# Performance work log

Measured on AMD Instinct MI355X. Metric: run time of the kernel, lower is better.

The kernel has to match this reference:

```python
import jax, jax.numpy as jnp
import numpy as np

D, H, HD, F, A, P, NB, MD = 1024, 16, 64, 2816, 64, 30, 32, 128
B, L = 4, 1024


def _rel_bucket(rel, num_buckets=NB, max_distance=MD):
    # T5 relative position bucket, bidirectional=False (decoder self-attn)
    rel = -jnp.minimum(rel, 0)
    max_exact = num_buckets // 2
    is_small = rel < max_exact
    large = max_exact + (
        jnp.log(jnp.maximum(rel, 1).astype(jnp.float32) / max_exact)
        / np.log(max_distance / max_exact)
        * (num_buckets - max_exact)
    ).astype(jnp.int32)
    large = jnp.minimum(large, num_buckets - 1)
    return jnp.where(is_small, rel, large)


def _rmsnorm(x, scale, eps=1e-6):
    var = jnp.mean(jnp.square(x), axis=-1, keepdims=True)
    return x * jax.lax.rsqrt(var + eps) * scale


def _attn(x, kv, wq, wk, wv, wo, mask, bias, pk, pv):
    # x: [B,Lq,D], kv: [B,Lk,D], prefix pk/pv: [B,P,H,HD]
    hd = wq.shape[-1]
    q = jnp.einsum('bqd,dhe->bqhe', x, wq) * (hd ** -0.5)
    k = jnp.einsum('bkd,dhe->bkhe', kv, wk)
    v = jnp.einsum('bkd,dhe->bkhe', kv, wv)
    k = jnp.concatenate([pk, k], axis=1)  # prefix KV prepended
    v = jnp.concatenate([pv, v], axis=1)
    logits = jnp.einsum('bqhe,bkhe->bhqk', q, k).astype(jnp.float32)
    p = pk.shape[1]
    if bias is not None:
        logits = logits + jnp.pad(bias, ((0, 0), (0, 0), (0, 0), (p, 0)))
    mask = jnp.pad(mask, ((0, 0), (0, 0), (0, 0), (p, 0)), constant_values=True)
    logits = jnp.where(mask, logits, jnp.float32(-1e10))
    w = jax.nn.softmax(logits, axis=-1).astype(x.dtype)
    o = jnp.einsum('bhqk,bkhe->bqhe', w, v)
    return jnp.einsum('bqhe,hed->bqd', o, wo)


def setup_inputs() -> dict:
    key = jax.random.key(0)
    ks = jax.random.split(key, 24)
    s = D ** -0.5
    inp = {
        'inputs': jax.random.normal(ks[0], (B, L, D), jnp.float32),
        'encoded': jax.random.normal(ks[1], (B, L, D), jnp.float32),
        'adapter_wd': jax.random.normal(ks[2], (B, D, A), jnp.float32) * s,
        'adapter_wu': jax.random.normal(ks[3], (B, A, D), jnp.float32) * (A ** -0.5),
        'adapter_bd': jax.random.normal(ks[4], (B, A), jnp.float32) * 0.02,
        'adapter_bu': jax.random.normal(ks[5], (B, D), jnp.float32) * 0.02,
        'prefix_key': jax.random.normal(ks[6], (B, 2, P, H, HD), jnp.float32),
        'prefix_value': jax.random.normal(ks[7], (B, 2, P, H, HD), jnp.float32),
        'ln1': jnp.ones((D,), jnp.float32),
        'ln2': jnp.ones((D,), jnp.float32),
        'ln3': jnp.ones((D,), jnp.float32),
        'sa_wq': jax.random.normal(ks[8], (D, H, HD), jnp.float32) * s,
        'sa_wk': jax.random.normal(ks[9], (D, H, HD), jnp.float32) * s,
        'sa_wv': jax.random.normal(ks[10], (D, H, HD), jnp.float32) * s,
        'sa_wo': jax.random.normal(ks[11], (H, HD, D), jnp.float32) * s,
        'ca_wq': jax.random.normal(ks[12], (D, H, HD), jnp.float32) * s,
        'ca_wk': jax.random.normal(ks[13], (D, H, HD), jnp.float32) * s,
        'ca_wv': jax.random.normal(ks[14], (D, H, HD), jnp.float32) * s,
        'ca_wo': jax.random.normal(ks[15], (H, HD, D), jnp.float32) * s,
        'relpos': jax.random.normal(ks[16], (H, NB), jnp.float32) * 0.1,
        'mlp_wi0': jax.random.normal(ks[17], (D, F), jnp.float32) * s,
        'mlp_wi1': jax.random.normal(ks[18], (D, F), jnp.float32) * s,
        'mlp_wo': jax.random.normal(ks[19], (F, D), jnp.float32) * (F ** -0.5),
        'decoder_mask': jnp.broadcast_to(jnp.tril(jnp.ones((L, L), bool))[None, None], (B, 1, L, L)),
        'encoder_decoder_mask': jnp.ones((B, 1, L, L), bool),
    }
    return inp


def reference(inputs, encoded, adapter_wd, adapter_wu, adapter_bd, adapter_bu,
              prefix_key, prefix_value, ln1, ln2, ln3,
              sa_wq, sa_wk, sa_wv, sa_wo, ca_wq, ca_wk, ca_wv, ca_wo,
              relpos, mlp_wi0, mlp_wi1, mlp_wo,
              decoder_mask, encoder_decoder_mask):
    l = inputs.shape[1]
    pos = jnp.arange(l)
    buckets = _rel_bucket(pos[None, :] - pos[:, None])  # [L,L]
    bias = relpos[:, buckets][None]                      # [1,H,L,L]
    # self-attention with prefix + relative bias
    x = _rmsnorm(inputs, ln1)
    x = _attn(x, x, sa_wq, sa_wk, sa_wv, sa_wo, decoder_mask, bias,
              prefix_key[:, 0], prefix_value[:, 0])
    x = x + inputs
    # cross-attention with prefix
    y = _rmsnorm(x, ln2)
    y = _attn(y, encoded, ca_wq, ca_wk, ca_wv, ca_wo, encoder_decoder_mask, None,
              prefix_key[:, 1], prefix_value[:, 1])
    y = y + x
    # gated-gelu MLP + per-example adapter
    lz = _rmsnorm(y, ln3)
    z = (jax.nn.gelu(lz @ mlp_wi0) * (lz @ mlp_wi1)) @ mlp_wo
    az = jnp.einsum('bld,bda->bla', lz, adapter_wd) + adapter_bd[:, None]
    az = jax.nn.gelu(az)
    az = jnp.einsum('bla,bad->bld', az, adapter_wu) + adapter_bu[:, None]
    z = z + az
    return z + y
```

## Files before the change

kernel.cpp:

```cpp
#include <hip/hip_runtime.h>

typedef unsigned short u16;
typedef __attribute__((ext_vector_type(8))) __bf16 bf16x8;
typedef __attribute__((ext_vector_type(4))) float f32x4;

__device__ __forceinline__ float bf2f(u16 u) {
  union { unsigned int i; float f; } v; v.i = ((unsigned int)u) << 16; return v.f;
}
__device__ __forceinline__ u16 f2bf(float f) {
  unsigned int x = __float_as_uint(f);
  unsigned int r = (x + 0x7fffu + ((x >> 16) & 1u)) >> 16;
  return (u16)r;
}
__device__ __forceinline__ u16 f2bf_fast(float f) {
  return (u16)((__float_as_uint(f) + 0x8000u) >> 16);
}
__device__ __forceinline__ float gelu_f(float x) {
  float u = 0.7978845608028654f * (x + 0.044715f * x * x * x);
  float t = 1.0f - 2.0f / (__expf(2.0f * u) + 1.0f);
  return 0.5f * x * (1.0f + t);
}
__device__ __forceinline__ void gl_lds16(const u16* g, u16* l) {
  __builtin_amdgcn_global_load_lds(
      (const __attribute__((address_space(1))) unsigned int*)g,
      (__attribute__((address_space(3))) unsigned int*)l, 16, 0, 0);
}

__global__ __launch_bounds__(256) void cast_bf16_k(const float* __restrict__ in,
                                                   u16* __restrict__ out, int n4) {
  int i = blockIdx.x * 256 + threadIdx.x;
  if (i >= n4) return;
  float4 v = ((const float4*)in)[i];
  ushort4 o;
  o.x = f2bf(v.x); o.y = f2bf(v.y); o.z = f2bf(v.z); o.w = f2bf(v.w);
  ((ushort4*)out)[i] = o;
}

__global__ __launch_bounds__(256) void transpose_k(
    const float* __restrict__ in, u16* __restrict__ out, int R, int C,
    long isb, long osb, int rs, int roff) {
  __shared__ u16 tile[32][33];
  in += (size_t)blockIdx.z * isb;
  out += (size_t)blockIdx.z * osb;
  int c0 = blockIdx.x * 32, r0 = blockIdx.y * 32;
  int tx = threadIdx.x & 31, ty = threadIdx.x >> 5;
#pragma unroll
  for (int i = 0; i < 4; ++i) {
    int rr = r0 + ty + i * 8;
    if (rr < R && c0 + tx < C) tile[ty + i * 8][tx] = f2bf(in[(size_t)rr * C + c0 + tx]);
  }
  __syncthreads();
#pragma unroll
  for (int i = 0; i < 4; ++i) {
    int cc = c0 + ty + i * 8;
    if (cc < C && r0 + tx < R)
      out[(size_t)(cc * rs + roff) * R + r0 + tx] = tile[tx][ty + i * 8];
  }
}

__global__ __launch_bounds__(256) void bias_tab_k(const float* __restrict__ relpos,
                                                  float* __restrict__ tab) {
  int idx = blockIdx.x * 256 + threadIdx.x;
  int h = idx >> 10, d = idx & 1023;
  int bucket;
  if (d < 16) bucket = d;
  else {
    int lb = 16 + (int)(logf((float)d * (1.0f / 16.0f)) * (16.0f / logf(8.0f)));
    bucket = lb < 31 ? lb : 31;
  }
  tab[idx] = relpos[h * 32 + bucket];
}

__global__ __launch_bounds__(256) void prefix_fill_k(
    const float* __restrict__ pK, const float* __restrict__ pV,
    u16* __restrict__ Kd, u16* __restrict__ Vtd, int sSel) {
  int idx = blockIdx.x * 256 + threadIdx.x;
  int e = idx & 63, p = (idx >> 6) & 31, h = (idx >> 11) & 15, b = idx >> 15;
  int key = (p < 30) ? p : (1024 + p);
  float kv = 0.f, vv = 0.f;
  if (p < 30) {
    size_t src = ((((size_t)(b * 2 + sSel)) * 30 + p) * 16 + h) * 64 + e;
    kv = pK[src]; vv = pV[src];
  }
  Kd[(((size_t)(b * 16 + h)) * 1056 + key) * 64 + e] = f2bf(kv);
  Vtd[(((size_t)(b * 16 + h)) * 64 + e) * 1056 + key] = f2bf(vv);
}

__global__ __launch_bounds__(256) void rmsnorm_k(const float* __restrict__ in,
                                                 const float* __restrict__ scale,
                                                 u16* __restrict__ out) {
  const int D = 1024;
  size_t base = (size_t)blockIdx.x * D;
  int t = threadIdx.x;
  float x[4];
#pragma unroll
  for (int i = 0; i < 4; ++i) x[i] = in[base + t + i * 256];
  float s = x[0] * x[0] + x[1] * x[1] + x[2] * x[2] + x[3] * x[3];
#pragma unroll
  for (int off = 1; off < 64; off <<= 1) s += __shfl_xor(s, off, 64);
  __shared__ float ws4[4];
  if ((t & 63) == 0) ws4[t >> 6] = s;
  __syncthreads();
  float tot = ws4[0] + ws4[1] + ws4[2] + ws4[3];
  float r = rsqrtf(tot * (1.0f / D) + 1e-6f);
#pragma unroll
  for (int i = 0; i < 4; ++i) {
    int c = t + i * 256;
    out[base + c] = f2bf(x[i] * r * scale[c]);
  }
}

__global__ __launch_bounds__(256) void rmsnorm_sum_k(
    const float* __restrict__ in0, const float* __restrict__ in1,
    const float* __restrict__ res, const float* __restrict__ scale,
    u16* __restrict__ outn, float* __restrict__ outs) {
  const int D = 1024;
  size_t base = (size_t)blockIdx.x * D;
  int t = threadIdx.x;
  float x[4];
#pragma unroll
  for (int i = 0; i < 4; ++i) {
    int c = t + i * 256;
    x[i] = in0[base + c] + in1[base + c] + res[base + c];
    outs[base + c] = x[i];
  }
  float s = x[0] * x[0] + x[1] * x[1] + x[2] * x[2] + x[3] * x[3];
#pragma unroll
  for (int off = 1; off < 64; off <<= 1) s += __shfl_xor(s, off, 64);
  __shared__ float ws4[4];
  if ((t & 63) == 0) ws4[t >> 6] = s;
  __syncthreads();
  float tot = ws4[0] + ws4[1] + ws4[2] + ws4[3];
  float r = rsqrtf(tot * (1.0f / D) + 1e-6f);
#pragma unroll
  for (int i = 0; i < 4; ++i) {
    int c = t + i * 256;
    outn[base + c] = f2bf(x[i] * r * scale[c]);
  }
}

template <int MODE>
__global__ __launch_bounds__(256) void gemm97(
    const u16* __restrict__ A, const u16* __restrict__ Bt, void* __restrict__ out,
    void* __restrict__ out2, void* __restrict__ out3,
    const float* __restrict__ res1, int M, int N, int K, int Ks, float alpha) {
  const int BK = 32;
  __shared__ __align__(16) u16 As[128 * 32];
  __shared__ __align__(16) u16 Bs[128 * 32];

  const int t = threadIdx.x;
  const int wave = t >> 6, lane = t & 63;
  int m0, n0;
  if (MODE != 13) {
    int wgid = blockIdx.y * gridDim.x + blockIdx.x;
    const int cpx = (gridDim.x * gridDim.y) >> 3;
    wgid = (wgid & 7) * cpx + (wgid >> 3);
    m0 = (wgid / gridDim.x) * 128;
    n0 = (wgid % gridDim.x) * 128;
  } else {
    m0 = blockIdx.y * 128;
    n0 = blockIdx.x * 128;
  }
  const int kbase = blockIdx.z * Ks;
  const int fr = lane & 15, fq = lane >> 4;
  const int wm = (wave >> 1) * 64, wn = (wave & 1) * 64;

  const int srow = wave * 32 + (lane >> 2);
  const int scol = (lane & 3) * 8;
  const u16* ag0 = A + (size_t)(m0 + srow) * K + kbase + scol;
  const u16* ag1 = ag0 + (size_t)16 * K;
  const u16* bg0 = Bt + (size_t)(n0 + srow) * K + kbase + scol;
  const u16* bg1 = bg0 + (size_t)16 * K;
  u16* al0 = &As[(wave * 32) * 32];
  u16* al1 = &As[(wave * 32 + 16) * 32];
  u16* bl0 = &Bs[(wave * 32) * 32];
  u16* bl1 = &Bs[(wave * 32 + 16) * 32];

  f32x4 acc[16];
#pragma unroll
  for (int i = 0; i < 16; ++i) acc[i] = (f32x4){0.f, 0.f, 0.f, 0.f};

  for (int k0 = 0; k0 < Ks; k0 += BK) {
    gl_lds16(ag0 + k0, al0);
    gl_lds16(ag1 + k0, al1);
    gl_lds16(bg0 + k0, bl0);
    gl_lds16(bg1 + k0, bl1);
    __syncthreads();
    bf16x8 af[4], bf[4];
#pragma unroll
    for (int i = 0; i < 4; ++i)
      af[i] = *(const bf16x8*)&As[(wm + i * 16 + fr) * 32 + fq * 8];
#pragma unroll
    for (int j = 0; j < 4; ++j)
      bf[j] = *(const bf16x8*)&Bs[(wn + j * 16 + fr) * 32 + fq * 8];
#pragma unroll
    for (int i = 0; i < 4; ++i)
#pragma unroll
      for (int j = 0; j < 4; ++j)
        acc[i * 4 + j] = __builtin_amdgcn_mfma_f32_16x16x32_bf16(
            af[i], bf[j], acc[i * 4 + j], 0, 0, 0);
    __syncthreads();
  }

#pragma unroll
  for (int i = 0; i < 4; ++i) {
#pragma unroll
    for (int rr = 0; rr < 4; ++rr) {
      long gm = (long)m0 + wm + i * 16 + fq * 4 + rr;
#pragma unroll
      for (int j = 0; j < 4; ++j) {
        int gn = n0 + wn + j * 16 + fr;
        float v = acc[i * 4 + j][rr];
        size_t oi = (size_t)gm * N + gn;
        if (MODE == 1) {
          float* po = blockIdx.z ? (float*)out2 : (float*)out;
          po[oi] = v;
        }
        if (MODE == 2) ((u16*)out)[oi] = f2bf(v);
        if (MODE == 8) {
          int b = (int)(gm >> 10), l = (int)(gm & 1023), h = gn >> 6, e = gn & 63;
          ((u16*)out)[(((size_t)(b * 16 + h)) * 1024 + l) * 64 + e] = f2bf(v * alpha);
        }
        if (MODE == 11) {
          int b = (int)(gm >> 10), l = (int)(gm & 1023);
          int sec = gn >> 10, nn = gn & 1023, h = nn >> 6, e = nn & 63;
          if (sec == 0)
            ((u16*)out)[(((size_t)(b * 16 + h)) * 1024 + l) * 64 + e] = f2bf(v * alpha);
          else if (sec == 1)
            ((u16*)out2)[(((size_t)(b * 16 + h)) * 1056 + 30 + l) * 64 + e] = f2bf(v);
          else
            ((u16*)out3)[(((size_t)(b * 16 + h)) * 64 + e) * 1056 + 30 + l] = f2bf(v);
        }
        if (MODE == 12) {
          int b = (int)(gm >> 10), l = (int)(gm & 1023);
          int sec = gn >> 10, nn = gn & 1023, h = nn >> 6, e = nn & 63;
          if (sec == 0)
            ((u16*)out)[(((size_t)(b * 16 + h)) * 1056 + 30 + l) * 64 + e] = f2bf(v);
          else
            ((u16*)out2)[(((size_t)(b * 16 + h)) * 64 + e) * 1056 + 30 + l] = f2bf(v);
        }
        if (MODE == 13) {
          float vo = __shfl_xor(v, 1, 64);
          if (!(fr & 1))
            ((u16*)out)[(size_t)gm * 2816 + (gn >> 1)] = f2bf(gelu_f(v) * vo);
        }
      }
    }
  }
}

template <int MODE>
__global__ __launch_bounds__(256) void gemm_bt(
    const u16* __restrict__ A, const u16* __restrict__ Bt, void* __restrict__ out,
    const float* __restrict__ res1, const float* __restrict__ res2,
    const float* __restrict__ res3, const float* __restrict__ bias,
    int M, int N, int K,
    long Asb, long Bsb, long bsb, long r1sb, long r2sb, long r3sb, long osb) {
  const int BM = 128, BK = 32, LP = 40;
  __shared__ __align__(16) u16 As[BM * LP];
  __shared__ __align__(16) u16 Bs[BM * LP];

  const int t = threadIdx.x;
  const int m0 = blockIdx.y * BM;
  const int n0 = blockIdx.x * 128;
  const int bz = blockIdx.z;
  A += (size_t)bz * Asb;
  Bt += (size_t)bz * Bsb;

  f32x4 acc[16];
#pragma unroll
  for (int i = 0; i < 16; ++i) acc[i] = (f32x4){0.f, 0.f, 0.f, 0.f};
  const int wave = t >> 6, lane = t & 63;
  const int wm = (wave >> 1) * 64, wn = (wave & 1) * 64;
  const int fr = lane & 15, fq = lane >> 4;

  for (int k0 = 0; k0 < K; k0 += BK) {
#pragma unroll
    for (int i = 0; i < 2; ++i) {
      int idx = (i * 256 + t) * 8;
      int row = idx >> 5, col = idx & 31;
      *(uint4*)&As[row * LP + col] =
          *(const uint4*)(A + (size_t)(m0 + row) * K + k0 + col);
      uint4 bv = {0u, 0u, 0u, 0u};
      if (n0 + row < N) bv = *(const uint4*)(Bt + (size_t)(n0 + row) * K + k0 + col);
      *(uint4*)&Bs[row * LP + col] = bv;
    }
    __syncthreads();
    bf16x8 af[4], bfr[4];
#pragma unroll
    for (int i = 0; i < 4; ++i)
      af[i] = *(const bf16x8*)&As[(wm + i * 16 + fr) * LP + fq * 8];
#pragma unroll
    for (int j = 0; j < 4; ++j)
      bfr[j] = *(const bf16x8*)&Bs[(wn + j * 16 + fr) * LP + fq * 8];
#pragma unroll
    for (int i = 0; i < 4; ++i)
#pragma unroll
      for (int j = 0; j < 4; ++j)
        acc[i * 4 + j] = __builtin_amdgcn_mfma_f32_16x16x32_bf16(
            af[i], bfr[j], acc[i * 4 + j], 0, 0, 0);
    __syncthreads();
  }

#pragma unroll
  for (int i = 0; i < 4; ++i) {
#pragma unroll
    for (int rr = 0; rr < 4; ++rr) {
      long gm = (long)m0 + wm + i * 16 + fq * 4 + rr;
#pragma unroll
      for (int j = 0; j < 4; ++j) {
        int gn = n0 + wn + j * 16 + fr;
        if (gn >= N) continue;
        float v = acc[i * 4 + j][rr];
        size_t oi = (size_t)bz * osb + (size_t)gm * N + gn;
        size_t ri = (size_t)gm * N + gn;
        if (MODE == 6) ((u16*)out)[oi] = f2bf(gelu_f(v + bias[(size_t)bz * bsb + gn]));
        if (MODE == 7)
          ((float*)out)[oi] = v + bias[(size_t)bz * bsb + gn] +
                              res1[(size_t)bz * r1sb + ri] +
                              res2[(size_t)bz * r2sb + ri] +
                              res3[(size_t)bz * r3sb + ri];
      }
    }
  }
}

template <bool IS_SELF>
__global__ __launch_bounds__(256) void fattn_k(
    const u16* __restrict__ Qg, const u16* __restrict__ Kg,
    const u16* __restrict__ Vtg, const float* __restrict__ bias_tab,
    u16* __restrict__ Out) {
  const int L = 1024, P = 30, KC = 1056;
  const int flat = blockIdx.x;
  const int wg = (flat & 7) * 64 + (flat >> 3);
  const int q0b = (wg & 7) * 128;
  const int h = (wg >> 3) & 15, b = wg >> 7;
  const int t = threadIdx.x, wave = t >> 6, lane = t & 63;
  const int fr = lane & 15, fq = lane >> 4;
  const int q0w = q0b + wave * 32;

  __shared__ float bTs[IS_SELF ? 1024 : 4];
  __shared__ __align__(16) u16 Ps[4][32][40];

  if (IS_SELF) {
#pragma unroll
    for (int i = 0; i < 4; ++i) bTs[t + i * 256] = bias_tab[h * 1024 + t + i * 256];
    __syncthreads();
  }

  const u16* qptr = Qg + (((size_t)(b * 16 + h)) * L + q0w + fr) * 64 + fq * 8;
  bf16x8 qa0 = *(const bf16x8*)qptr;
  bf16x8 qa1 = *(const bf16x8*)(qptr + 32);
  bf16x8 qb0 = *(const bf16x8*)(qptr + 16 * 64);
  bf16x8 qb1 = *(const bf16x8*)(qptr + 16 * 64 + 32);

  f32x4 oA[4], oB[4];
#pragma unroll
  for (int i = 0; i < 4; ++i) {
    oA[i] = (f32x4){0.f, 0.f, 0.f, 0.f};
    oB[i] = (f32x4){0.f, 0.f, 0.f, 0.f};
  }
  f32x4 olA = (f32x4){0.f, 0.f, 0.f, 0.f};
  f32x4 olB = (f32x4){0.f, 0.f, 0.f, 0.f};
  bf16x8 ones;
  {
    u16 one = 0x3F80;
#pragma unroll
    for (int i = 0; i < 8; ++i) ((u16*)&ones)[i] = one;
  }

  const int nk = IS_SELF ? (P + q0b + 128) : (P + L);
  const int nch = (nk + 31) >> 5;
  const u16* kp = Kg + ((size_t)(b * 16 + h)) * KC * 64 + (size_t)fr * 64 + fq * 8;
  const u16* vp = Vtg + ((size_t)(b * 16 + h)) * 64 * KC + (size_t)fr * KC + fq * 8;

  bf16x8 kf0 = *(const bf16x8*)(kp + 0);
  bf16x8 kf1 = *(const bf16x8*)(kp + 32);
  bf16x8 kf2 = *(const bf16x8*)(kp + 16 * 64);
  bf16x8 kf3 = *(const bf16x8*)(kp + 16 * 64 + 32);

  auto smax = [&](f32x4* s, int k0, int qoff, int rb) {
    const bool full = IS_SELF ? (k0 >= 32 && k0 + 31 - P <= qoff)
                              : (k0 + 31 < P + L);
    if (full) {
      if (IS_SELF) {
#pragma unroll
        for (int reg = 0; reg < 4; ++reg) {
          const int qq = qoff + fq * 4 + reg;
          s[0][reg] += bTs[qq - (k0 + fr - P)];
          s[1][reg] += bTs[qq - (k0 + 16 + fr - P)];
        }
      }
    } else {
#pragma unroll
      for (int reg = 0; reg < 4; ++reg) {
        const int qq = qoff + fq * 4 + reg;
#pragma unroll
        for (int t2 = 0; t2 < 2; ++t2) {
          const int kvi = k0 + t2 * 16 + fr;
          float sv = s[t2][reg];
          if (IS_SELF) {
            const int lk = kvi - P;
            if (lk >= 0) {
              if (lk <= qq) sv += bTs[qq - lk];
              else sv = -3.0e38f;
            }
          } else {
            if (kvi >= P + L) sv = -3.0e38f;
          }
          s[t2][reg] = sv;
        }
      }
    }
#pragma unroll
    for (int reg = 0; reg < 4; ++reg) {
      Ps[wave][rb + fq * 4 + reg][fr] = f2bf_fast(__expf(s[0][reg]));
      Ps[wave][rb + fq * 4 + reg][16 + fr] = f2bf_fast(__expf(s[1][reg]));
    }
  };

  for (int ch = 0; ch < nch; ++ch) {
    const int k0 = ch * 32;
    bf16x8 vf0 = *(const bf16x8*)(vp + 0 * 16 * KC + k0);
    bf16x8 vf1 = *(const bf16x8*)(vp + 1 * 16 * KC + k0);
    bf16x8 vf2 = *(const bf16x8*)(vp + 2 * 16 * KC + k0);
    bf16x8 vf3 = *(const bf16x8*)(vp + 3 * 16 * KC + k0);
    const int k0n = (ch + 1 < nch) ? (k0 + 32) : 0;
    bf16x8 kn0 = *(const bf16x8*)(kp + (size_t)k0n * 64);
    bf16x8 kn1 = *(const bf16x8*)(kp + (size_t)k0n * 64 + 32);
    bf16x8 kn2 = *(const bf16x8*)(kp + (size_t)(k0n + 16) * 64);
    bf16x8 kn3 = *(const bf16x8*)(kp + (size_t)(k0n + 16) * 64 + 32);

    f32x4 sA[2], sB[2];
    sA[0] = (f32x4){0.f, 0.f, 0.f, 0.f};
    sA[1] = (f32x4){0.f, 0.f, 0.f, 0.f};
    sB[0] = (f32x4){0.f, 0.f, 0.f, 0.f};
    sB[1] = (f32x4){0.f, 0.f, 0.f, 0.f};
    sA[0] = __builtin_amdgcn_mfma_f32_16x16x32_bf16(qa0, kf0, sA[0], 0, 0, 0);
    sA[0] = __builtin_amdgcn_mfma_f32_16x16x32_bf16(qa1, kf1, sA[0], 0, 0, 0);
    sA[1] = __builtin_amdgcn_mfma_f32_16x16x32_bf16(qa0, kf2, sA[1], 0, 0, 0);
    sA[1] = __builtin_amdgcn_mfma_f32_16x16x32_bf16(qa1, kf3, sA[1], 0, 0, 0);
    sB[0] = __builtin_amdgcn_mfma_f32_16x16x32_bf16(qb0, kf0, sB[0], 0, 0, 0);
    sB[0] = __builtin_amdgcn_mfma_f32_16x16x32_bf16(qb1, kf1, sB[0], 0, 0, 0);
    sB[1] = __builtin_amdgcn_mfma_f32_16x16x32_bf16(qb0, kf2, sB[1], 0, 0, 0);
    sB[1] = __builtin_amdgcn_mfma_f32_16x16x32_bf16(qb1, kf3, sB[1], 0, 0, 0);

    smax(sA, k0, q0w, 0);
    smax(sB, k0, q0w + 16, 16);
    __asm__ volatile("s_waitcnt lgkmcnt(0)" ::: "memory");
    bf16x8 paA = *(const bf16x8*)&Ps[wave][fr][fq * 8];
    bf16x8 paB = *(const bf16x8*)&Ps[wave][16 + fr][fq * 8];

    oA[0] = __builtin_amdgcn_mfma_f32_16x16x32_bf16(paA, vf0, oA[0], 0, 0, 0);
    oA[1] = __builtin_amdgcn_mfma_f32_16x16x32_bf16(paA, vf1, oA[1], 0, 0, 0);
    oA[2] = __builtin_amdgcn_mfma_f32_16x16x32_bf16(paA, vf2, oA[2], 0, 0, 0);
    oA[3] = __builtin_amdgcn_mfma_f32_16x16x32_bf16(paA, vf3, oA[3], 0, 0, 0);
    olA   = __builtin_amdgcn_mfma_f32_16x16x32_bf16(paA, ones, olA, 0, 0, 0);
    oB[0] = __builtin_amdgcn_mfma_f32_16x16x32_bf16(paB, vf0, oB[0], 0, 0, 0);
    oB[1] = __builtin_amdgcn_mfma_f32_16x16x32_bf16(paB, vf1, oB[1], 0, 0, 0);
    oB[2] = __builtin_amdgcn_mfma_f32_16x16x32_bf16(paB, vf2, oB[2], 0, 0, 0);
    oB[3] = __builtin_amdgcn_mfma_f32_16x16x32_bf16(paB, vf3, oB[3], 0, 0, 0);
    olB   = __builtin_amdgcn_mfma_f32_16x16x32_bf16(paB, ones, olB, 0, 0, 0);

    kf0 = kn0; kf1 = kn1; kf2 = kn2; kf3 = kn3;
  }

  float invA[4], invB[4];
#pragma unroll
  for (int reg = 0; reg < 4; ++reg) {
    invA[reg] = 1.0f / olA[reg];
    invB[reg] = 1.0f / olB[reg];
  }
#pragma unroll
  for (int dt = 0; dt < 4; ++dt) {
#pragma unroll
    for (int reg = 0; reg < 4; ++reg) {
      size_t rowA = (size_t)(b * L + q0w + fq * 4 + reg);
      Out[(rowA * 16 + h) * 64 + dt * 16 + fr] = f2bf(oA[dt][reg] * invA[reg]);
      size_t rowB = rowA + 16;
      Out[(rowB * 16 + h) * 64 + dt * 16 + fr] = f2bf(oB[dt][reg] * invB[reg]);
    }
  }
}

extern "C" void kernel_launch(void* const* d_in, const int* in_sizes, int n_in,
                              void* d_out, int out_size, void* d_ws, size_t ws_size,
                              hipStream_t stream) {
  const int B = 4, L = 1024, D = 1024, H = 16, F = 2816, AD = 64;
  const int M = B * L;
  const int KC = 1056;

  const float* inputs  = (const float*)d_in[0];
  const float* encoded = (const float*)d_in[1];
  const float* a_wd    = (const float*)d_in[2];
  const float* a_wu    = (const float*)d_in[3];
  const float* a_bd    = (const float*)d_in[4];
  const float* a_bu    = (const float*)d_in[5];
  const float* pK      = (const float*)d_in[6];
  const float* pV      = (const float*)d_in[7];
  const float* ln1     = (const float*)d_in[8];
  const float* ln2     = (const float*)d_in[9];
  const float* ln3     = (const float*)d_in[10];
  const float* sa_wq   = (const float*)d_in[11];
  const float* sa_wk   = (const float*)d_in[12];
  const float* sa_wv   = (const float*)d_in[13];
  const float* sa_wo   = (const float*)d_in[14];
  const float* ca_wq   = (const float*)d_in[15];
  const float* ca_wk   = (const float*)d_in[16];
  const float* ca_wv   = (const float*)d_in[17];
  const float* ca_wo   = (const float*)d_in[18];
  const float* relpos  = (const float*)d_in[19];
  const float* wi0     = (const float*)d_in[20];
  const float* wi1     = (const float*)d_in[21];
  const float* wom     = (const float*)d_in[22];

  char* w = (char*)d_ws;
  size_t used = 0;
  auto alloc = [&](size_t bytes) {
    char* p = w + used;
    used += (bytes + 255) & ~(size_t)255;
    return p;
  };
  u16* wqkvT  = (u16*)alloc((size_t)3072 * 1024 * 2);
  u16* woT    = (u16*)alloc((size_t)D * 1024 * 2);
  u16* cqT    = (u16*)alloc((size_t)D * 1024 * 2);
  u16* ckvT   = (u16*)alloc((size_t)2048 * 1024 * 2);
  u16* coT    = (u16*)alloc((size_t)D * 1024 * 2);
  u16* wi01T  = (u16*)alloc((size_t)5632 * 1024 * 2);
  u16* womT   = (u16*)alloc((size_t)D * F * 2);
  u16* wdT    = (u16*)alloc((size_t)B * AD * D * 2);
  u16* wuT    = (u16*)alloc((size_t)B * D * AD * 2);
  float* bT   = (float*)alloc((size_t)H * 1024 * 4);
  u16* enc16  = (u16*)alloc((size_t)M * D * 2);
  u16* xn     = (u16*)alloc((size_t)M * D * 2);
  u16* lz     = (u16*)alloc((size_t)M * D * 2);
  u16* Kc     = (u16*)alloc((size_t)B * H * KC * 64 * 2);
  u16* Vtc    = (u16*)alloc((size_t)B * H * 64 * KC * 2);
  u16* qh     = (u16*)alloc((size_t)B * H * L * 64 * 2);
  u16* ao     = (u16*)alloc((size_t)M * D * 2);
  float* xf   = (float*)alloc((size_t)M * D * 4);
  float* yf   = (float*)alloc((size_t)M * D * 4);
  u16* az1    = (u16*)alloc((size_t)B * 1024 * AD * 2);
  float* pk0  = (float*)Kc;
  u16* g      = Kc;
  float* zf0  = (float*)enc16;
  float* zf1  = (float*)ao;
  if (used > ws_size) return;

  dim3 tb(256);
  auto T = [&](const float* src, u16* dst, int R, int C, int nb, long sb,
               int rs, int roff) {
    transpose_k<<<dim3((C + 31) / 32, (R + 31) / 32, nb), tb, 0, stream>>>(
        src, dst, R, C, sb, sb, rs, roff);
  };
  T(sa_wq, wqkvT, D, 1024, 1, 0, 1, 0);
  T(sa_wk, wqkvT + (size_t)1024 * 1024, D, 1024, 1, 0, 1, 0);
  T(sa_wv, wqkvT + (size_t)2048 * 1024, D, 1024, 1, 0, 1, 0);
  T(sa_wo, woT, 1024, D, 1, 0, 1, 0);
  T(ca_wq, cqT, D, 1024, 1, 0, 1, 0);
  T(ca_wk, ckvT, D, 1024, 1, 0, 1, 0);
  T(ca_wv, ckvT + (size_t)1024 * 1024, D, 1024, 1, 0, 1, 0);
  T(ca_wo, coT, 1024, D, 1, 0, 1, 0);
  T(wi0, wi01T, D, F, 1, 0, 2, 0);
  T(wi1, wi01T, D, F, 1, 0, 2, 1);
  T(wom, womT, F, D, 1, 0, 1, 0);
  T(a_wd, wdT, D, AD, B, (long)D * AD, 1, 0);
  T(a_wu, wuT, AD, D, B, (long)AD * D, 1, 0);
  bias_tab_k<<<dim3(64), tb, 0, stream>>>(relpos, bT);
  cast_bf16_k<<<dim3(M * D / 4 / 256), tb, 0, stream>>>(encoded, enc16, M * D / 4);

#define G97(MODE, Ap, Btp, Op, O2, O3, R1, Nn, Kk, al)                         \
  gemm97<MODE><<<dim3((Nn) / 128, M / 128), tb, 0, stream>>>(                  \
      (const u16*)(Ap), (const u16*)(Btp), (void*)(Op), (void*)(O2),           \
      (void*)(O3), (const float*)(R1), M, Nn, Kk, Kk, al)

  rmsnorm_k<<<dim3(M), tb, 0, stream>>>(inputs, ln1, xn);
  G97(11, xn, wqkvT, qh, Kc, Vtc, nullptr, 3072, D, 0.125f);
  prefix_fill_k<<<dim3(512), tb, 0, stream>>>(pK, pV, Kc, Vtc, 0);
  fattn_k<true><<<dim3(512), tb, 0, stream>>>(qh, Kc, Vtc, bT, ao);
  gemm97<1><<<dim3(8, M / 128, 2), tb, 0, stream>>>(
      (const u16*)ao, (const u16*)woT, (void*)pk0, (void*)xf, nullptr,
      nullptr, M, 1024, 1024, 512, 1.f);
  rmsnorm_sum_k<<<dim3(M), tb, 0, stream>>>(pk0, xf, inputs, ln2, xn, xf);
  G97(8, xn, cqT, qh, nullptr, nullptr, nullptr, 1024, D, 0.125f);
  G97(12, enc16, ckvT, Kc, Vtc, nullptr, nullptr, 2048, D, 1.f);
  prefix_fill_k<<<dim3(512), tb, 0, stream>>>(pK, pV, Kc, Vtc, 1);
  fattn_k<false><<<dim3(512), tb, 0, stream>>>(qh, Kc, Vtc, nullptr, ao);
  gemm97<1><<<dim3(8, M / 128, 2), tb, 0, stream>>>(
      (const u16*)ao, (const u16*)coT, (void*)pk0, (void*)yf, nullptr,
      nullptr, M, 1024, 1024, 512, 1.f);
  rmsnorm_sum_k<<<dim3(M), tb, 0, stream>>>(pk0, yf, xf, ln3, lz, yf);
  gemm_bt<6><<<dim3(1, 8, B), tb, 0, stream>>>(
      lz, wdT, az1, nullptr, nullptr, nullptr, a_bd, 1024, AD, D,
      (long)1024 * D, (long)AD * D, (long)AD, 0, 0, 0, (long)1024 * AD);
  gemm97<13><<<dim3(5632 / 128, M / 128), tb, 0, stream>>>(
      (const u16*)lz, (const u16*)wi01T, (void*)g, nullptr, nullptr,
      nullptr, M, 5632, 1024, 1024, 1.f);
  gemm97<1><<<dim3(8, M / 128, 2), tb, 0, stream>>>(
      (const u16*)g, (const u16*)womT, (void*)zf0, (void*)zf1, nullptr,
      nullptr, M, 1024, 2816, 1408, 1.f);
  gemm_bt<7><<<dim3(8, 8, B), tb, 0, stream>>>(
      az1, wuT, d_out, zf0, zf1, yf, a_bu, 1024, 1024, AD,
      (long)1024 * AD, (long)D * AD, (long)1024, (long)1024 * 1024,
      (long)1024 * 1024, (long)1024 * 1024, (long)1024 * 1024);
#undef G97
  (void)in_sizes; (void)n_in; (void)out_size;
}
```

Before: 713.8 us.

## Batch weight transposes, fuse cross-attn Q/KV GEMMs, restructure gated-MLP epilogue

Replaces eight separate attention-weight transpose launches with one batched launch over a pointer table, and transposes the MLP input weights in one launch. The wi0/wi1 interleave is changed to 16-row blocks, so the gated-GELU epilogue reads gate and linear values from adjacent accumulators and no longer needs a lane shuffle. The cross-attention Q and KV projections are merged into one GEMM launch that picks its A operand per column block. Launch overhead drops, the merged GEMM fills more of the GPU, and some epilogue work goes away. The cost is that the weight layout coupling between the transpose and the MLP epilogue must stay consistent. Swizzling is now limited to MODE 1.

After: 713.8 us. Within noise of the previous version (+0.0%).

```diff
diff --git a/kernel.cpp b/kernel.cpp
--- a/kernel.cpp
+++ b/kernel.cpp
@@ -53,8 +53,36 @@
 #pragma unroll
   for (int i = 0; i < 4; ++i) {
     int cc = c0 + ty + i * 8;
-    if (cc < C && r0 + tx < R)
-      out[(size_t)(cc * rs + roff) * R + r0 + tx] = tile[tx][ty + i * 8];
+    if (cc < C && r0 + tx < R) {
+      int orow = (((cc >> 4) * rs + roff) << 4) + (cc & 15);
+      out[(size_t)orow * R + r0 + tx] = tile[tx][ty + i * 8];
+    }
+  }
+}
+
+struct TSrc8 { const float* p[8]; };
+__global__ __launch_bounds__(256) void transpose8_k(
+    TSrc8 srcs, u16* __restrict__ out, int R, int C,
+    long zstride, int rs, int roffz) {
+  __shared__ u16 tile[32][33];
+  const float* __restrict__ in = srcs.p[blockIdx.z];
+  out += (size_t)blockIdx.z * zstride;
+  const int roff = roffz ? blockIdx.z : 0;
+  int c0 = blockIdx.x * 32, r0 = blockIdx.y * 32;
+  int tx = threadIdx.x & 31, ty = threadIdx.x >> 5;
+#pragma unroll
+  for (int i = 0; i < 4; ++i) {
+    int rr = r0 + ty + i * 8;
+    if (rr < R && c0 + tx < C) tile[ty + i * 8][tx] = f2bf(in[(size_t)rr * C + c0 + tx]);
+  }
+  __syncthreads();
+#pragma unroll
+  for (int i = 0; i < 4; ++i) {
+    int cc = c0 + ty + i * 8;
+    if (cc < C && r0 + tx < R) {
+      int orow = (((cc >> 4) * rs + roff) << 4) + (cc & 15);
+      out[(size_t)orow * R + r0 + tx] = tile[tx][ty + i * 8];
+    }
   }
 }
 
@@ -141,9 +169,10 @@
 
 template <int MODE>
 __global__ __launch_bounds__(256) void gemm97(
-    const u16* __restrict__ A, const u16* __restrict__ Bt, void* __restrict__ out,
+    const u16* __restrict__ A, const u16* __restrict__ A2,
+    const u16* __restrict__ Bt, void* __restrict__ out,
     void* __restrict__ out2, void* __restrict__ out3,
-    const float* __restrict__ res1, int M, int N, int K, int Ks, float alpha) {
+    int M, int N, int K, int Ks, float alpha) {
   const int BK = 32;
   __shared__ __align__(16) u16 As[128 * 32];
   __shared__ __align__(16) u16 Bs[128 * 32];
@@ -151,7 +180,7 @@
   const int t = threadIdx.x;
   const int wave = t >> 6, lane = t & 63;
   int m0, n0;
-  if (MODE != 13) {
+  if (MODE == 1) {
     int wgid = blockIdx.y * gridDim.x + blockIdx.x;
     const int cpx = (gridDim.x * gridDim.y) >> 3;
     wgid = (wgid & 7) * cpx + (wgid >> 3);
@@ -165,9 +194,10 @@
   const int fr = lane & 15, fq = lane >> 4;
   const int wm = (wave >> 1) * 64, wn = (wave & 1) * 64;
 
+  const u16* Ause = (MODE == 14 && n0 >= 1024) ? A2 : A;
   const int srow = wave * 32 + (lane >> 2);
   const int scol = (lane & 3) * 8;
-  const u16* ag0 = A + (size_t)(m0 + srow) * K + kbase + scol;
+  const u16* ag0 = Ause + (size_t)(m0 + srow) * K + kbase + scol;
   const u16* ag1 = ag0 + (size_t)16 * K;
   const u16* bg0 = Bt + (size_t)(n0 + srow) * K + kbase + scol;
   const u16* bg1 = bg0 + (size_t)16 * K;
@@ -207,6 +237,16 @@
 #pragma unroll
     for (int rr = 0; rr < 4; ++rr) {
       long gm = (long)m0 + wm + i * 16 + fq * 4 + rr;
+      if (MODE == 13) {
+#pragma unroll
+        for (int p = 0; p < 2; ++p) {
+          float gate = acc[i * 4 + 2 * p][rr];
+          float lin = acc[i * 4 + 2 * p + 1][rr];
+          int col = ((n0 + wn) >> 1) + p * 16 + fr;
+          ((u16*)out)[(size_t)gm * 2816 + col] = f2bf(gelu_f(gate) * lin);
+        }
+        continue;
+      }
 #pragma unroll
       for (int j = 0; j < 4; ++j) {
         int gn = n0 + wn + j * 16 + fr;
@@ -216,12 +256,11 @@
           float* po = blockIdx.z ? (float*)out2 : (float*)out;
           po[oi] = v;
         }
-        if (MODE == 2) ((u16*)out)[oi] = f2bf(v);
         if (MODE == 8) {
           int b = (int)(gm >> 10), l = (int)(gm & 1023), h = gn >> 6, e = gn & 63;
           ((u16*)out)[(((size_t)(b * 16 + h)) * 1024 + l) * 64 + e] = f2bf(v * alpha);
         }
-        if (MODE == 11) {
+        if (MODE == 11 || MODE == 14) {
           int b = (int)(gm >> 10), l = (int)(gm & 1023);
           int sec = gn >> 10, nn = gn & 1023, h = nn >> 6, e = nn & 63;
           if (sec == 0)
@@ -230,19 +269,6 @@
             ((u16*)out2)[(((size_t)(b * 16 + h)) * 1056 + 30 + l) * 64 + e] = f2bf(v);
           else
             ((u16*)out3)[(((size_t)(b * 16 + h)) * 64 + e) * 1056 + 30 + l] = f2bf(v);
-        }
-        if (MODE == 12) {
-          int b = (int)(gm >> 10), l = (int)(gm & 1023);
-          int sec = gn >> 10, nn = gn & 1023, h = nn >> 6, e = nn & 63;
-          if (sec == 0)
-            ((u16*)out)[(((size_t)(b * 16 + h)) * 1056 + 30 + l) * 64 + e] = f2bf(v);
-          else
-            ((u16*)out2)[(((size_t)(b * 16 + h)) * 64 + e) * 1056 + 30 + l] = f2bf(v);
-        }
-        if (MODE == 13) {
-          float vo = __shfl_xor(v, 1, 64);
-          if (!(fr & 1))
-            ((u16*)out)[(size_t)gm * 2816 + (gn >> 1)] = f2bf(gelu_f(v) * vo);
         }
       }
     }
@@ -548,61 +574,50 @@
   if (used > ws_size) return;
 
   dim3 tb(256);
-  auto T = [&](const float* src, u16* dst, int R, int C, int nb, long sb,
-               int rs, int roff) {
-    transpose_k<<<dim3((C + 31) / 32, (R + 31) / 32, nb), tb, 0, stream>>>(
-        src, dst, R, C, sb, sb, rs, roff);
-  };
-  T(sa_wq, wqkvT, D, 1024, 1, 0, 1, 0);
-  T(sa_wk, wqkvT + (size_t)1024 * 1024, D, 1024, 1, 0, 1, 0);
-  T(sa_wv, wqkvT + (size_t)2048 * 1024, D, 1024, 1, 0, 1, 0);
-  T(sa_wo, woT, 1024, D, 1, 0, 1, 0);
-  T(ca_wq, cqT, D, 1024, 1, 0, 1, 0);
-  T(ca_wk, ckvT, D, 1024, 1, 0, 1, 0);
-  T(ca_wv, ckvT + (size_t)1024 * 1024, D, 1024, 1, 0, 1, 0);
-  T(ca_wo, coT, 1024, D, 1, 0, 1, 0);
-  T(wi0, wi01T, D, F, 1, 0, 2, 0);
-  T(wi1, wi01T, D, F, 1, 0, 2, 1);
-  T(wom, womT, F, D, 1, 0, 1, 0);
-  T(a_wd, wdT, D, AD, B, (long)D * AD, 1, 0);
-  T(a_wu, wuT, AD, D, B, (long)AD * D, 1, 0);
+  TSrc8 s8;
+  s8.p[0] = sa_wq; s8.p[1] = sa_wk; s8.p[2] = sa_wv; s8.p[3] = sa_wo;
+  s8.p[4] = ca_wq; s8.p[5] = ca_wk; s8.p[6] = ca_wv; s8.p[7] = ca_wo;
+  transpose8_k<<<dim3(32, 32, 8), tb, 0, stream>>>(
+      s8, wqkvT, 1024, 1024, (long)1024 * 1024, 1, 0);
+  TSrc8 swi;
+  swi.p[0] = wi0; swi.p[1] = wi1;
+  for (int i = 2; i < 8; ++i) swi.p[i] = wi0;
+  transpose8_k<<<dim3(88, 32, 2), tb, 0, stream>>>(
+      swi, wi01T, 1024, 2816, 0, 2, 1);
+  transpose_k<<<dim3(32, 88, 1), tb, 0, stream>>>(
+      wom, womT, 2816, 1024, 0, 0, 1, 0);
+  transpose_k<<<dim3(2, 32, B), tb, 0, stream>>>(
+      a_wd, wdT, D, AD, (long)D * AD, (long)D * AD, 1, 0);
+  transpose_k<<<dim3(32, 2, B), tb, 0, stream>>>(
+      a_wu, wuT, AD, D, (long)AD * D, (long)AD * D, 1, 0);
   bias_tab_k<<<dim3(64), tb, 0, stream>>>(relpos, bT);
   cast_bf16_k<<<dim3(M * D / 4 / 256), tb, 0, stream>>>(encoded, enc16, M * D / 4);
 
-#define G97(MODE, Ap, Btp, Op, O2, O3, R1, Nn, Kk, al)                         \
-  gemm97<MODE><<<dim3((Nn) / 128, M / 128), tb, 0, stream>>>(                  \
-      (const u16*)(Ap), (const u16*)(Btp), (void*)(Op), (void*)(O2),           \
-      (void*)(O3), (const float*)(R1), M, Nn, Kk, Kk, al)
-
   rmsnorm_k<<<dim3(M), tb, 0, stream>>>(inputs, ln1, xn);
-  G97(11, xn, wqkvT, qh, Kc, Vtc, nullptr, 3072, D, 0.125f);
+  gemm97<11><<<dim3(24, 32), tb, 0, stream>>>(
+      xn, nullptr, wqkvT, qh, Kc, Vtc, M, 3072, 1024, 1024, 0.125f);
   prefix_fill_k<<<dim3(512), tb, 0, stream>>>(pK, pV, Kc, Vtc, 0);
   fattn_k<true><<<dim3(512), tb, 0, stream>>>(qh, Kc, Vtc, bT, ao);
-  gemm97<1><<<dim3(8, M / 128, 2), tb, 0, stream>>>(
-      (const u16*)ao, (const u16*)woT, (void*)pk0, (void*)xf, nullptr,
-      nullptr, M, 1024, 1024, 512, 1.f);
+  gemm97<1><<<dim3(8, 32, 2), tb, 0, stream>>>(
+      ao, nullptr, woT, pk0, xf, nullptr, M, 1024, 1024, 512, 1.f);
   rmsnorm_sum_k<<<dim3(M), tb, 0, stream>>>(pk0, xf, inputs, ln2, xn, xf);
-  G97(8, xn, cqT, qh, nullptr, nullptr, nullptr, 1024, D, 0.125f);
-  G97(12, enc16, ckvT, Kc, Vtc, nullptr, nullptr, 2048, D, 1.f);
+  gemm97<14><<<dim3(24, 32), tb, 0, stream>>>(
+      xn, enc16, cqT, qh, Kc, Vtc, M, 3072, 1024, 1024, 0.125f);
   prefix_fill_k<<<dim3(512), tb, 0, stream>>>(pK, pV, Kc, Vtc, 1);
   fattn_k<false><<<dim3(512), tb, 0, stream>>>(qh, Kc, Vtc, nullptr, ao);
-  gemm97<1><<<dim3(8, M / 128, 2), tb, 0, stream>>>(
-      (const u16*)ao, (const u16*)coT, (void*)pk0, (void*)yf, nullptr,
-      nullptr, M, 1024, 1024, 512, 1.f);
+  gemm97<1><<<dim3(8, 32, 2), tb, 0, stream>>>(
+      ao, nullptr, coT, pk0, yf, nullptr, M, 1024, 1024, 512, 1.f);
   rmsnorm_sum_k<<<dim3(M), tb, 0, stream>>>(pk0, yf, xf, ln3, lz, yf);
   gemm_bt<6><<<dim3(1, 8, B), tb, 0, stream>>>(
       lz, wdT, az1, nullptr, nullptr, nullptr, a_bd, 1024, AD, D,
       (long)1024 * D, (long)AD * D, (long)AD, 0, 0, 0, (long)1024 * AD);
-  gemm97<13><<<dim3(5632 / 128, M / 128), tb, 0, stream>>>(
-      (const u16*)lz, (const u16*)wi01T, (void*)g, nullptr, nullptr,
-      nullptr, M, 5632, 1024, 1024, 1.f);
-  gemm97<1><<<dim3(8, M / 128, 2), tb, 0, stream>>>(
-      (const u16*)g, (const u16*)womT, (void*)zf0, (void*)zf1, nullptr,
-      nullptr, M, 1024, 2816, 1408, 1.f);
+  gemm97<13><<<dim3(44, 32), tb, 0, stream>>>(
+      lz, nullptr, wi01T, g, nullptr, nullptr, M, 5632, 1024, 1024, 1.f);
+  gemm97<1><<<dim3(8, 32, 2), tb, 0, stream>>>(
+      g, nullptr, womT, zf0, zf1, nullptr, M, 1024, 2816, 1408, 1.f);
   gemm_bt<7><<<dim3(8, 8, B), tb, 0, stream>>>(
       az1, wuT, d_out, zf0, zf1, yf, a_bu, 1024, 1024, AD,
       (long)1024 * AD, (long)D * AD, (long)1024, (long)1024 * 1024,
       (long)1024 * 1024, (long)1024 * 1024, (long)1024 * 1024);
-#undef G97
   (void)in_sizes; (void)n_in; (void)out_size;
 }
```
